# Kernel tuning notes

Hardware: AMD Instinct MI355X
Metric: run time of the kernel (lower is better)

## Reference

```python
import jax, jax.numpy as jnp
import numpy as np

B, L, C, H, RATIO = 2, 512, 256, 8, 4
D = C // H
EPS = 1e-5


def layernorm(x, g, b):
    m = jnp.mean(x, axis=-1, keepdims=True)
    v = jnp.mean((x - m) ** 2, axis=-1, keepdims=True)
    return (x - m) * jax.lax.rsqrt(v + EPS) * g + b


def setup_inputs() -> dict:
    key = jax.random.key(0)
    ks = jax.random.split(key, 10)
    s = 0.02
    return {
        "x": jax.random.normal(ks[0], (B, L, C), jnp.float32),
        "relative_pos": jax.random.normal(ks[1], (B, L, L, C), jnp.float32),
        # attention params (qkv_bias=False)
        "w_qkv": jax.random.normal(ks[2], (C, 3 * C), jnp.float32) * s,
        "w_proj": jax.random.normal(ks[3], (C, C), jnp.float32) * s,
        "b_proj": jnp.zeros((C,), jnp.float32),
        # relative_project: Linear(C,H) -> GELU -> LayerNorm(H)
        "w_rel": jax.random.normal(ks[4], (C, H), jnp.float32) * s,
        "b_rel": jnp.zeros((H,), jnp.float32),
        "g_reln": jnp.ones((H,), jnp.float32),
        "b_reln": jnp.zeros((H,), jnp.float32),
        # block layernorms
        "g_n1": jnp.ones((C,), jnp.float32),
        "b_n1": jnp.zeros((C,), jnp.float32),
        "g_n2": jnp.ones((C,), jnp.float32),
        "b_n2": jnp.zeros((C,), jnp.float32),
        # MLP (mlp_ratio=4, act=GELU)
        "w_mlp1": jax.random.normal(ks[5], (C, RATIO * C), jnp.float32) * s,
        "b_mlp1": jnp.zeros((RATIO * C,), jnp.float32),
        "w_mlp2": jax.random.normal(ks[6], (RATIO * C, C), jnp.float32) * s,
        "b_mlp2": jnp.zeros((C,), jnp.float32),
    }


def reference(x, relative_pos, w_qkv, w_proj, b_proj, w_rel, b_rel,
              g_reln, b_reln, g_n1, b_n1, g_n2, b_n2,
              w_mlp1, b_mlp1, w_mlp2, b_mlp2):
    # eval mode: dropout / droppath are identity
    scale = D ** -0.5

    # --- attention branch ---
    h = layernorm(x, g_n1, b_n1)                      # [B,L,C]
    qkv = (h @ w_qkv).reshape(B, L, 3, H, D)
    qkv = jnp.transpose(qkv, (2, 0, 3, 1, 4))          # [3,B,H,L,D]
    q, k, v = qkv[0], qkv[1], qkv[2]

    attn = jnp.einsum("bhid,bhjd->bhij", q, k)        # [B,H,L,L]

    # relative bias: Linear -> GELU(exact) -> LayerNorm over heads
    rel = jax.nn.gelu(relative_pos @ w_rel + b_rel, approximate=False)  # [B,L,L,H]
    rel = layernorm(rel, g_reln, b_reln)
    rel = jnp.transpose(rel, (0, 3, 1, 2))            # [B,H,L,L]

    attn = jax.nn.softmax((attn + rel) * scale, axis=-1)
    o = jnp.einsum("bhij,bhjd->bhid", attn, v)        # [B,H,L,D]
    o = jnp.transpose(o, (0, 2, 1, 3)).reshape(B, L, C)
    o = o @ w_proj + b_proj
    x = x + o

    # --- MLP branch (jump=False since out_feat==in_feat) ---
    h = layernorm(x, g_n2, b_n2)
    h = jax.nn.gelu(h @ w_mlp1 + b_mlp1, approximate=False)
    h = h @ w_mlp2 + b_mlp2
    return x + h
```

## Files before the change

### kernel.cpp

```cpp
#include <hip/hip_runtime.h>
#include <hip/hip_bf16.h>
#include <cstddef>

#define EPS_ 1e-5f
#define SCALE_ 0.1767766952966369f

typedef short bf16x8_t __attribute__((ext_vector_type(8)));
typedef float f32x4_t  __attribute__((ext_vector_type(4)));

__device__ __forceinline__ float gelu_f(float x) {
    float y = 0.7978845608028654f * (x + 0.044715f * x * x * x);
    float e = __expf(2.0f * y);
    float t = 1.0f - 2.0f * __builtin_amdgcn_rcpf(e + 1.0f);
    return 0.5f * x * (1.0f + t);
}
__device__ __forceinline__ unsigned short f2bf(float f) {
    return __builtin_bit_cast(unsigned short, __float2bfloat16(f));
}
__device__ __forceinline__ unsigned f2bf2(float a, float b) {
    unsigned lo = __builtin_bit_cast(unsigned short, __float2bfloat16(a));
    unsigned hi = __builtin_bit_cast(unsigned short, __float2bfloat16(b));
    return lo | (hi << 16);
}
__device__ __forceinline__ float bf2f(unsigned short s) {
    unsigned u = (unsigned)s << 16;
    return __builtin_bit_cast(float, u);
}

__device__ __forceinline__ void ln_row_body(const float* __restrict__ x,
                                            const float* __restrict__ g,
                                            const float* __restrict__ b,
                                            unsigned short* __restrict__ out,
                                            int row, int lane) {
    const float4 xv = *(const float4*)(x + (size_t)row * 256 + lane * 4);
    float s  = xv.x + xv.y + xv.z + xv.w;
    float sq = xv.x*xv.x + xv.y*xv.y + xv.z*xv.z + xv.w*xv.w;
#pragma unroll
    for (int m = 1; m < 64; m <<= 1) { s += __shfl_xor(s, m); sq += __shfl_xor(sq, m); }
    float mean = s * (1.0f/256.0f);
    float var  = sq * (1.0f/256.0f) - mean*mean;
    float rstd = rsqrtf(var + EPS_);
    float4 gv = *(const float4*)(g + lane*4);
    float4 bv = *(const float4*)(b + lane*4);
    uint2 o;
    o.x = f2bf2((xv.x-mean)*rstd*gv.x + bv.x, (xv.y-mean)*rstd*gv.y + bv.y);
    o.y = f2bf2((xv.z-mean)*rstd*gv.z + bv.z, (xv.w-mean)*rstd*gv.w + bv.w);
    *(uint2*)(out + (size_t)row * 256 + lane * 4) = o;
}

__global__ __launch_bounds__(256) void prep_kernel(
    const float* __restrict__ w_qkv,  unsigned short* __restrict__ wqkvT,
    const float* __restrict__ w_mlp1, unsigned short* __restrict__ wmlp1T,
    const float* __restrict__ w_mlp2, unsigned short* __restrict__ wmlp2T,
    const float* __restrict__ w_proj, unsigned short* __restrict__ wprojbf,
    const float* __restrict__ x, const float* __restrict__ g_n1,
    const float* __restrict__ b_n1, unsigned short* __restrict__ hbf) {
    __shared__ float tile[32][33];
    int bid = blockIdx.x, t = threadIdx.x;
    if (bid >= 768) {
        ln_row_body(x, g_n1, b_n1, hbf, (bid - 768) * 4 + (t >> 6), t & 63);
        return;
    }
    if (bid >= 704) {
        int idx = (bid - 704) * 256 + t;
        float4 v = ((const float4*)w_proj)[idx];
        uint2 o;
        o.x = f2bf2(v.x, v.y);
        o.y = f2bf2(v.z, v.w);
        *(uint2*)(wprojbf + (size_t)idx * 4) = o;
        return;
    }
    const float* W; unsigned short* WT; int K, N, tt;
    if (bid < 192)      { W = w_qkv;  WT = wqkvT;  K = 256;  N = 768;  tt = bid; }
    else if (bid < 448) { W = w_mlp1; WT = wmlp1T; K = 256;  N = 1024; tt = bid - 192; }
    else                { W = w_mlp2; WT = wmlp2T; K = 1024; N = 256;  tt = bid - 448; }
    int ntn = N >> 5;
    int kt = tt / ntn, nt = tt % ntn;
    int k0 = kt * 32, n0 = nt * 32;
    {
        int kr = t >> 3, cg = (t & 7) * 4;
        float4 v = *(const float4*)(W + (size_t)(k0 + kr) * N + n0 + cg);
        tile[kr][cg+0] = v.x; tile[kr][cg+1] = v.y; tile[kr][cg+2] = v.z; tile[kr][cg+3] = v.w;
    }
    __syncthreads();
    {
        int nr = t >> 3, kg = (t & 7) * 4;
        uint2 o;
        o.x = f2bf2(tile[kg+0][nr], tile[kg+1][nr]);
        o.y = f2bf2(tile[kg+2][nr], tile[kg+3][nr]);
        *(uint2*)(WT + (size_t)(n0 + nr) * K + k0 + kg) = o;
    }
}

template<bool BIAS, bool GACT, bool BF16OUT, int KSPLIT, bool ATOMIC, bool VOUT>
__global__ __launch_bounds__(256) void mgemm_kernel(
    const unsigned short* __restrict__ A, const unsigned short* __restrict__ BT,
    const float* __restrict__ bias,
    void* __restrict__ Cout, unsigned short* __restrict__ vbf, int M, int N, int K) {
    __shared__ unsigned short Al[64][40];
    __shared__ unsigned short Bl[64][40];
    int t = threadIdx.x;
    int bm = blockIdx.x, bn = blockIdx.y, kz = blockIdx.z;
    int kchunk = K / KSPLIT;
    int srow = t >> 2, skk = (t & 3) * 8;
    const unsigned short* Ap = A  + (size_t)(bm*64 + srow) * K + kz*kchunk + skk;
    const unsigned short* Bp = BT + (size_t)(bn*64 + srow) * K + kz*kchunk + skk;
    int lane = t & 63, w = t >> 6, wr = w >> 1, wc = w & 1;
    int fr = lane & 15, fg = lane >> 4;
    f32x4_t a00 = {0.f,0.f,0.f,0.f}, a01 = {0.f,0.f,0.f,0.f};
    f32x4_t a10 = {0.f,0.f,0.f,0.f}, a11 = {0.f,0.f,0.f,0.f};
    for (int kk = 0; kk < kchunk; kk += 32) {
        uint4 av = *(const uint4*)(Ap + kk);
        uint4 bv = *(const uint4*)(Bp + kk);
        __syncthreads();
        *(uint4*)&Al[srow][skk] = av;
        *(uint4*)&Bl[srow][skk] = bv;
        __syncthreads();
        bf16x8_t fa0 = *(const bf16x8_t*)&Al[wr*32      + fr][fg*8];
        bf16x8_t fa1 = *(const bf16x8_t*)&Al[wr*32 + 16 + fr][fg*8];
        bf16x8_t fb0 = *(const bf16x8_t*)&Bl[wc*32      + fr][fg*8];
        bf16x8_t fb1 = *(const bf16x8_t*)&Bl[wc*32 + 16 + fr][fg*8];
        a00 = __builtin_amdgcn_mfma_f32_16x16x32_bf16(fa0, fb0, a00, 0, 0, 0);
        a01 = __builtin_amdgcn_mfma_f32_16x16x32_bf16(fa0, fb1, a01, 0, 0, 0);
        a10 = __builtin_amdgcn_mfma_f32_16x16x32_bf16(fa1, fb0, a10, 0, 0, 0);
        a11 = __builtin_amdgcn_mfma_f32_16x16x32_bf16(fa1, fb1, a11, 0, 0, 0);
    }
    float* Cf = (float*)Cout;
    unsigned short* Cb = (unsigned short*)Cout;
    auto emit = [&](f32x4_t acc, int mi, int ni) {
        int Ro = bm*64 + wr*32 + mi*16 + fg*4;
        int Co = bn*64 + wc*32 + ni*16 + fr;
        float bval = BIAS ? bias[Co] : 0.f;
#pragma unroll
        for (int e = 0; e < 4; ++e) {
            int r = Ro + e;
            float v = acc[e];
            if (BIAS)  v += bval;
            if (GACT)  v = gelu_f(v);
            if (ATOMIC)      atomicAdd(&Cf[(size_t)r * N + Co], v);
            else if (BF16OUT) Cb[(size_t)r * N + Co] = f2bf(v);
            else              Cf[(size_t)r * N + Co] = v;
            if (VOUT && Co >= 512) vbf[(size_t)r * 256 + (Co - 512)] = f2bf(v);
        }
    };
    emit(a00, 0, 0); emit(a01, 0, 1); emit(a10, 1, 0); emit(a11, 1, 1);
}

__global__ __launch_bounds__(256) void qk_kernel(const float* __restrict__ qkv,
                                                 unsigned short* __restrict__ qk) {
    __shared__ float k_lds[512*32];
    int t = threadIdx.x;
    int it = blockIdx.x;
    int h  = blockIdx.y;
    int b  = blockIdx.z;
    const float* base = qkv + (size_t)b * 393216;
#pragma unroll
    for (int r = 0; r < 16; ++r) {
        int idx = r*256 + t;
        int row = idx >> 3, c4 = idx & 7;
        float4 kv = *(const float4*)(base + (size_t)row*768 + 256 + h*32 + c4*4);
        *(float4*)(k_lds + row*32 + c4*4) = kv;
    }
    __syncthreads();
    int ir = t & 31, jg = t >> 5;
    int i = it*32 + ir;
    float4 q[8];
    const float* qp = base + (size_t)i*768 + h*32;
#pragma unroll
    for (int c4 = 0; c4 < 8; ++c4) q[c4] = *(const float4*)(qp + c4*4);
    unsigned short* outp = qk + (((size_t)(b*512 + i))*8 + h)*512 + jg*64;
    for (int jj = 0; jj < 64; jj += 4) {
        float a4[4];
#pragma unroll
        for (int u = 0; u < 4; ++u) {
            const float* kp = k_lds + (size_t)(jg*64 + jj + u)*32;
            float acc = 0.f;
#pragma unroll
            for (int c4 = 0; c4 < 8; ++c4) {
                float4 kv = *(const float4*)(kp + c4*4);
                acc += q[c4].x*kv.x + q[c4].y*kv.y + q[c4].z*kv.z + q[c4].w*kv.w;
            }
            a4[u] = acc;
        }
        uint2 o2;
        o2.x = f2bf2(a4[0], a4[1]);
        o2.y = f2bf2(a4[2], a4[3]);
        *(uint2*)(outp + jj) = o2;
    }
}

#define LGS 520
__global__ __launch_bounds__(256) void rel_mega_kernel(
    const float* __restrict__ rp, const unsigned short* __restrict__ qk,
    const unsigned short* __restrict__ vbf,
    const float* __restrict__ w_rel, const float* __restrict__ b_rel,
    const float* __restrict__ g_reln, const float* __restrict__ b_reln,
    const unsigned short* __restrict__ wprojbf, const float* __restrict__ b_proj,
    const float* __restrict__ x, const float* __restrict__ g_n2,
    const float* __restrict__ b_n2, const float* __restrict__ b_mlp2,
    float* __restrict__ out, unsigned short* __restrict__ h2bf) {
    __shared__ float lg_lds[8*LGS];
    __shared__ float o_lds[256];
    __shared__ float red[8];
    int t = threadIdx.x;
    int bi = blockIdx.x;
    int b  = bi >> 9;
    int wid = t >> 6, lane = t & 63;
    int fr = lane & 15, fg = lane >> 4;
    bool act = fr < 8;
    bf16x8_t bfrag[8];
#pragma unroll
    for (int kk = 0; kk < 8; ++kk) {
        bf16x8_t bf;
#pragma unroll
        for (int e = 0; e < 8; ++e) {
            float v = act ? w_rel[(size_t)(kk*32 + fg*8 + e)*8 + fr] : 0.f;
            bf[e] = (short)f2bf(v);
        }
        bfrag[kk] = bf;
    }
    const float* rpb = rp + (size_t)bi * 512 * 256;
#pragma unroll 1
    for (int tile = 0; tile < 8; ++tile) {
        int j0 = wid*128 + tile*16;
        const float* arow = rpb + (size_t)(j0 + fr)*256 + fg*8;
        f32x4_t acc = {0.f,0.f,0.f,0.f};
#pragma unroll
        for (int kk = 0; kk < 8; ++kk) {
            float4 x0 = *(const float4*)(arow + kk*32);
            float4 x1 = *(const float4*)(arow + kk*32 + 4);
            union { bf16x8_t v; uint4 u; } cvt;
            cvt.u.x = f2bf2(x0.x, x0.y);
            cvt.u.y = f2bf2(x0.z, x0.w);
            cvt.u.z = f2bf2(x1.x, x1.y);
            cvt.u.w = f2bf2(x1.z, x1.w);
            acc = __builtin_amdgcn_mfma_f32_16x16x32_bf16(cvt.v, bfrag[kk], acc, 0, 0, 0);
        }
        if (act) {
#pragma unroll
            for (int r = 0; r < 4; ++r)
                lg_lds[fr*LGS + j0 + fg*4 + r] = acc[r];
        }
    }
    __syncthreads();
#pragma unroll
    for (int rep = 0; rep < 2; ++rep) {
        int j = t + rep*256;
        float gv[8];
        float sm = 0.f, sq = 0.f;
#pragma unroll
        for (int h = 0; h < 8; ++h) {
            float val = lg_lds[h*LGS + j] + b_rel[h];
            float g = gelu_f(val);
            gv[h] = g; sm += g; sq += g*g;
        }
        float mean = sm * 0.125f;
        float var  = sq * 0.125f - mean*mean;
        float rstd = rsqrtf(var + EPS_);
#pragma unroll
        for (int h = 0; h < 8; ++h)
            lg_lds[h*LGS + j] = (gv[h] - mean) * rstd * g_reln[h] + b_reln[h];
    }
    __syncthreads();
    {
        int h = wid*2 + (lane >> 5);
        int sub = lane & 31;
        float* row = lg_lds + h*LGS;
        const unsigned short* qrow = qk + ((size_t)bi*8 + h)*512;
        float v[16];
#pragma unroll
        for (int c4 = 0; c4 < 4; ++c4) {
            float4 r4 = *(const float4*)(row + c4*128 + sub*4);
            ushort4 q4 = *(const ushort4*)(qrow + c4*128 + sub*4);
            v[c4*4+0] = (bf2f(q4.x) + r4.x) * SCALE_;
            v[c4*4+1] = (bf2f(q4.y) + r4.y) * SCALE_;
            v[c4*4+2] = (bf2f(q4.z) + r4.z) * SCALE_;
            v[c4*4+3] = (bf2f(q4.w) + r4.w) * SCALE_;
        }
        float mx = v[0];
#pragma unroll
        for (int e = 1; e < 16; ++e) mx = fmaxf(mx, v[e]);
#pragma unroll
        for (int m = 1; m < 32; m <<= 1) mx = fmaxf(mx, __shfl_xor(mx, m));
        float s = 0.f;
#pragma unroll
        for (int e = 0; e < 16; ++e) { v[e] = __expf(v[e] - mx); s += v[e]; }
#pragma unroll
        for (int m = 1; m < 32; m <<= 1) s += __shfl_xor(s, m);
        float inv = 1.0f / s;
#pragma unroll
        for (int e = 0; e < 16; ++e) v[e] *= inv;
#pragma unroll
        for (int c4 = 0; c4 < 4; ++c4) {
            float4 o4 = make_float4(v[c4*4+0], v[c4*4+1], v[c4*4+2], v[c4*4+3]);
            *(float4*)(row + c4*128 + sub*4) = o4;
        }
    }
    __syncthreads();
    {
        int c = t, h = c >> 5;
        const unsigned short* vcol = vbf + (size_t)b*131072 + c;
        const float* arow = lg_lds + h*LGS;
        float acc = 0.f;
        for (int j = 0; j < 512; j += 4) {
            float4 a4 = *(const float4*)(arow + j);
            acc += a4.x * bf2f(vcol[(size_t)(j+0)*256]);
            acc += a4.y * bf2f(vcol[(size_t)(j+1)*256]);
            acc += a4.z * bf2f(vcol[(size_t)(j+2)*256]);
            acc += a4.w * bf2f(vcol[(size_t)(j+3)*256]);
        }
        o_lds[c] = acc;
    }
    __syncthreads();
    float x1c;
    {
        int c = t;
        float acc2 = 0.f;
        for (int k = 0; k < 256; k += 4) {
            acc2 += o_lds[k+0] * bf2f(wprojbf[(size_t)(k+0)*256 + c]);
            acc2 += o_lds[k+1] * bf2f(wprojbf[(size_t)(k+1)*256 + c]);
            acc2 += o_lds[k+2] * bf2f(wprojbf[(size_t)(k+2)*256 + c]);
            acc2 += o_lds[k+3] * bf2f(wprojbf[(size_t)(k+3)*256 + c]);
        }
        x1c = x[(size_t)bi*256 + c] + b_proj[c] + acc2;
        out[(size_t)bi*256 + c] = x1c + b_mlp2[c];
    }
    {
        float s = x1c, sq = x1c*x1c;
#pragma unroll
        for (int m = 1; m < 64; m <<= 1) { s += __shfl_xor(s, m); sq += __shfl_xor(sq, m); }
        if (lane == 0) { red[wid*2] = s; red[wid*2+1] = sq; }
        __syncthreads();
        float S  = red[0] + red[2] + red[4] + red[6];
        float SQ = red[1] + red[3] + red[5] + red[7];
        float mean = S * (1.0f/256.0f);
        float var  = SQ * (1.0f/256.0f) - mean*mean;
        float rstd = rsqrtf(var + EPS_);
        float h2 = (x1c - mean) * rstd * g_n2[t] + b_n2[t];
        h2bf[(size_t)bi*256 + t] = f2bf(h2);
    }
}

extern "C" void kernel_launch(void* const* d_in, const int* in_sizes, int n_in,
                              void* d_out, int out_size, void* d_ws, size_t ws_size,
                              hipStream_t stream) {
    const float* x      = (const float*)d_in[0];
    const float* rp     = (const float*)d_in[1];
    const float* w_qkv  = (const float*)d_in[2];
    const float* w_proj = (const float*)d_in[3];
    const float* b_proj = (const float*)d_in[4];
    const float* w_rel  = (const float*)d_in[5];
    const float* b_rel  = (const float*)d_in[6];
    const float* g_reln = (const float*)d_in[7];
    const float* b_reln = (const float*)d_in[8];
    const float* g_n1   = (const float*)d_in[9];
    const float* b_n1   = (const float*)d_in[10];
    const float* g_n2   = (const float*)d_in[11];
    const float* b_n2   = (const float*)d_in[12];
    const float* w_mlp1 = (const float*)d_in[13];
    const float* b_mlp1 = (const float*)d_in[14];
    const float* w_mlp2 = (const float*)d_in[15];
    const float* b_mlp2 = (const float*)d_in[16];
    float* out = (float*)d_out;

    float* ws      = (float*)d_ws;
    float* ws_qkv  = ws;
    unsigned short* ub = (unsigned short*)(ws_qkv + 786432);
    unsigned short* qkbf    = ub;
    unsigned short* vbf     = qkbf + 4194304;
    unsigned short* hbf     = vbf  + 262144;
    unsigned short* h2bf    = hbf  + 262144;
    unsigned short* hgbf    = h2bf + 262144;
    unsigned short* wqkvT   = hgbf + 1048576;
    unsigned short* wmlp1T  = wqkvT + 196608;
    unsigned short* wmlp2T  = wmlp1T + 262144;
    unsigned short* wprojbf = wmlp2T + 262144;

    prep_kernel<<<1024, 256, 0, stream>>>(w_qkv, wqkvT, w_mlp1, wmlp1T, w_mlp2, wmlp2T,
                                          w_proj, wprojbf, x, g_n1, b_n1, hbf);
    mgemm_kernel<false,false,false,1,false,true><<<dim3(16,12,1), 256, 0, stream>>>(
        hbf, wqkvT, nullptr, ws_qkv, vbf, 1024, 768, 256);
    qk_kernel<<<dim3(16,8,2), 256, 0, stream>>>(ws_qkv, qkbf);
    rel_mega_kernel<<<1024, 256, 0, stream>>>(rp, qkbf, vbf, w_rel, b_rel,
                                              g_reln, b_reln, wprojbf, b_proj,
                                              x, g_n2, b_n2, b_mlp2, out, h2bf);
    mgemm_kernel<true,true,true,1,false,false><<<dim3(16,16,1), 256, 0, stream>>>(
        h2bf, wmlp1T, b_mlp1, hgbf, nullptr, 1024, 1024, 256);
    mgemm_kernel<false,false,false,4,true,false><<<dim3(16,4,4), 256, 0, stream>>>(
        hgbf, wmlp2T, nullptr, out, nullptr, 1024, 256, 1024);
}
```

Baseline: 184.8 us.

## Fuse both MLP GEMMs into one kernel keeping hidden activations in LDS

Replaces the two MLP GEMM launches (fc1 with bias+GELU to a bf16 workspace, then split-K fc2 with atomics) by a single kernel. Each block handles 16 rows: it computes the 1024-wide hidden layer into shared memory, then the fc2 product, and adds it into the output. This removes one launch, the hidden-activation round trip through global memory, and the atomics. In exchange only 64 blocks run, and B fragments are read straight from global memory with no LDS reuse, so parallelism and weight reuse drop.

```diff
diff --git a/kernel.cpp b/kernel.cpp
--- a/kernel.cpp
+++ b/kernel.cpp
@@ -92,24 +92,22 @@
     }
 }
 
-template<bool BIAS, bool GACT, bool BF16OUT, int KSPLIT, bool ATOMIC, bool VOUT>
+template<bool VOUT>
 __global__ __launch_bounds__(256) void mgemm_kernel(
     const unsigned short* __restrict__ A, const unsigned short* __restrict__ BT,
-    const float* __restrict__ bias,
     void* __restrict__ Cout, unsigned short* __restrict__ vbf, int M, int N, int K) {
     __shared__ unsigned short Al[64][40];
     __shared__ unsigned short Bl[64][40];
     int t = threadIdx.x;
-    int bm = blockIdx.x, bn = blockIdx.y, kz = blockIdx.z;
-    int kchunk = K / KSPLIT;
+    int bm = blockIdx.x, bn = blockIdx.y;
     int srow = t >> 2, skk = (t & 3) * 8;
-    const unsigned short* Ap = A  + (size_t)(bm*64 + srow) * K + kz*kchunk + skk;
-    const unsigned short* Bp = BT + (size_t)(bn*64 + srow) * K + kz*kchunk + skk;
+    const unsigned short* Ap = A  + (size_t)(bm*64 + srow) * K + skk;
+    const unsigned short* Bp = BT + (size_t)(bn*64 + srow) * K + skk;
     int lane = t & 63, w = t >> 6, wr = w >> 1, wc = w & 1;
     int fr = lane & 15, fg = lane >> 4;
     f32x4_t a00 = {0.f,0.f,0.f,0.f}, a01 = {0.f,0.f,0.f,0.f};
     f32x4_t a10 = {0.f,0.f,0.f,0.f}, a11 = {0.f,0.f,0.f,0.f};
-    for (int kk = 0; kk < kchunk; kk += 32) {
+    for (int kk = 0; kk < K; kk += 32) {
         uint4 av = *(const uint4*)(Ap + kk);
         uint4 bv = *(const uint4*)(Bp + kk);
         __syncthreads();
@@ -126,20 +124,14 @@
         a11 = __builtin_amdgcn_mfma_f32_16x16x32_bf16(fa1, fb1, a11, 0, 0, 0);
     }
     float* Cf = (float*)Cout;
-    unsigned short* Cb = (unsigned short*)Cout;
     auto emit = [&](f32x4_t acc, int mi, int ni) {
         int Ro = bm*64 + wr*32 + mi*16 + fg*4;
         int Co = bn*64 + wc*32 + ni*16 + fr;
-        float bval = BIAS ? bias[Co] : 0.f;
 #pragma unroll
         for (int e = 0; e < 4; ++e) {
             int r = Ro + e;
             float v = acc[e];
-            if (BIAS)  v += bval;
-            if (GACT)  v = gelu_f(v);
-            if (ATOMIC)      atomicAdd(&Cf[(size_t)r * N + Co], v);
-            else if (BF16OUT) Cb[(size_t)r * N + Co] = f2bf(v);
-            else              Cf[(size_t)r * N + Co] = v;
+            Cf[(size_t)r * N + Co] = v;
             if (VOUT && Co >= 512) vbf[(size_t)r * 256 + (Co - 512)] = f2bf(v);
         }
     };
@@ -338,6 +330,58 @@
         float rstd = rsqrtf(var + EPS_);
         float h2 = (x1c - mean) * rstd * g_n2[t] + b_n2[t];
         h2bf[(size_t)bi*256 + t] = f2bf(h2);
+    }
+}
+
+__global__ __launch_bounds__(256) void fused_mlp_kernel(
+    const unsigned short* __restrict__ h2bf,
+    const unsigned short* __restrict__ wmlp1T, const float* __restrict__ b_mlp1,
+    const unsigned short* __restrict__ wmlp2T,
+    float* __restrict__ out) {
+    __shared__ unsigned short h2s[16][264];
+    __shared__ unsigned short hgs[16][1032];
+    int t = threadIdx.x;
+    int bm = blockIdx.x;
+    int lane = t & 63, w = t >> 6;
+    int fr = lane & 15, fg = lane >> 4;
+#pragma unroll
+    for (int rep = 0; rep < 2; ++rep) {
+        int idx = (rep*256 + t) * 8;
+        int row = idx >> 8, col = idx & 255;
+        *(uint4*)&h2s[row][col] = *(const uint4*)(h2bf + (size_t)(bm*16 + row)*256 + col);
+    }
+    __syncthreads();
+#pragma unroll 1
+    for (int nt = 0; nt < 16; ++nt) {
+        int n0 = w*256 + nt*16;
+        f32x4_t acc = {0.f,0.f,0.f,0.f};
+#pragma unroll
+        for (int kk = 0; kk < 8; ++kk) {
+            bf16x8_t fa = *(const bf16x8_t*)&h2s[fr][kk*32 + fg*8];
+            bf16x8_t fb = *(const bf16x8_t*)(wmlp1T + (size_t)(n0 + fr)*256 + kk*32 + fg*8);
+            acc = __builtin_amdgcn_mfma_f32_16x16x32_bf16(fa, fb, acc, 0, 0, 0);
+        }
+        float bval = b_mlp1[n0 + fr];
+#pragma unroll
+        for (int e = 0; e < 4; ++e)
+            hgs[fg*4 + e][n0 + fr] = f2bf(gelu_f(acc[e] + bval));
+    }
+    __syncthreads();
+#pragma unroll 1
+    for (int ct = 0; ct < 4; ++ct) {
+        int c0 = w*64 + ct*16;
+        f32x4_t acc = {0.f,0.f,0.f,0.f};
+#pragma unroll 8
+        for (int kk = 0; kk < 32; ++kk) {
+            bf16x8_t fa = *(const bf16x8_t*)&hgs[fr][kk*32 + fg*8];
+            bf16x8_t fb = *(const bf16x8_t*)(wmlp2T + (size_t)(c0 + fr)*1024 + kk*32 + fg*8);
+            acc = __builtin_amdgcn_mfma_f32_16x16x32_bf16(fa, fb, acc, 0, 0, 0);
+        }
+#pragma unroll
+        for (int e = 0; e < 4; ++e) {
+            size_t off = (size_t)(bm*16 + fg*4 + e) * 256 + c0 + fr;
+            out[off] += acc[e];
+        }
     }
 }
 
@@ -370,22 +414,18 @@
     unsigned short* vbf     = qkbf + 4194304;
     unsigned short* hbf     = vbf  + 262144;
     unsigned short* h2bf    = hbf  + 262144;
-    unsigned short* hgbf    = h2bf + 262144;
-    unsigned short* wqkvT   = hgbf + 1048576;
+    unsigned short* wqkvT   = h2bf + 262144;
     unsigned short* wmlp1T  = wqkvT + 196608;
     unsigned short* wmlp2T  = wmlp1T + 262144;
     unsigned short* wprojbf = wmlp2T + 262144;
 
     prep_kernel<<<1024, 256, 0, stream>>>(w_qkv, wqkvT, w_mlp1, wmlp1T, w_mlp2, wmlp2T,
                                           w_proj, wprojbf, x, g_n1, b_n1, hbf);
-    mgemm_kernel<false,false,false,1,false,true><<<dim3(16,12,1), 256, 0, stream>>>(
-        hbf, wqkvT, nullptr, ws_qkv, vbf, 1024, 768, 256);
+    mgemm_kernel<true><<<dim3(16,12,1), 256, 0, stream>>>(
+        hbf, wqkvT, ws_qkv, vbf, 1024, 768, 256);
     qk_kernel<<<dim3(16,8,2), 256, 0, stream>>>(ws_qkv, qkbf);
     rel_mega_kernel<<<1024, 256, 0, stream>>>(rp, qkbf, vbf, w_rel, b_rel,
                                               g_reln, b_reln, wprojbf, b_proj,
                                               x, g_n2, b_n2, b_mlp2, out, h2bf);
-    mgemm_kernel<true,true,true,1,false,false><<<dim3(16,16,1), 256, 0, stream>>>(
-        h2bf, wmlp1T, b_mlp1, hgbf, nullptr, 1024, 1024, 256);
-    mgemm_kernel<false,false,false,4,true,false><<<dim3(16,4,4), 256, 0, stream>>>(
-        hgbf, wmlp2T, nullptr, out, nullptr, 1024, 256, 1024);
-}
+    fused_mlp_kernel<<<64, 256, 0, stream>>>(h2bf, wmlp1T, b_mlp1, wmlp2T, out);
+}
```

Result: slower. 211.3 us (+14.3%).
